# Kernel optimization log

Hardware: AMD Instinct MI355X
Metric: run time of the kernel (lower is better)

The kernel has to match this reference:

```python
import jax, jax.numpy as jnp
import numpy as np

D_MODEL, D_K, D_V, H, D_FF = 512, 64, 64, 8, 2048
B, N = 8, 1024
LN_EPS = 1e-5


def _layer_norm(x, g, b):
    mu = jnp.mean(x, axis=-1, keepdims=True)
    var = jnp.mean((x - mu) ** 2, axis=-1, keepdims=True)
    return (x - mu) * jax.lax.rsqrt(var + LN_EPS) * g + b


def setup_inputs() -> dict:
    key = jax.random.key(0)
    ks = jax.random.split(key, 16)
    s = 0.02
    return {
        "queries": jax.random.normal(ks[0], (B, N, D_MODEL), jnp.float32),
        "keys": jax.random.normal(ks[1], (B, N, D_MODEL), jnp.float32),
        "values": jax.random.normal(ks[2], (B, N, D_MODEL), jnp.float32),
        "relative_geometry_weights": jax.random.uniform(ks[3], (B, H, N, N), jnp.float32),
        "pos": jax.random.normal(ks[4], (B, N, D_MODEL), jnp.float32),
        "Wq": jax.random.normal(ks[5], (D_MODEL, H * D_K), jnp.float32) * s,
        "bq": jnp.zeros((H * D_K,), jnp.float32),
        "Wk": jax.random.normal(ks[6], (D_MODEL, H * D_K), jnp.float32) * s,
        "bk": jnp.zeros((H * D_K,), jnp.float32),
        "Wv": jax.random.normal(ks[7], (D_MODEL, H * D_V), jnp.float32) * s,
        "bv": jnp.zeros((H * D_V,), jnp.float32),
        "Wo": jax.random.normal(ks[8], (H * D_V, D_MODEL), jnp.float32) * s,
        "bo": jnp.zeros((D_MODEL,), jnp.float32),
        "ln1_g": jnp.ones((D_MODEL,), jnp.float32),
        "ln1_b": jnp.zeros((D_MODEL,), jnp.float32),
        "W1": jax.random.normal(ks[9], (D_MODEL, D_FF), jnp.float32) * s,
        "b1": jnp.zeros((D_FF,), jnp.float32),
        "W2": jax.random.normal(ks[10], (D_FF, D_MODEL), jnp.float32) * s,
        "b2": jnp.zeros((D_MODEL,), jnp.float32),
        "ln2_g": jnp.ones((D_MODEL,), jnp.float32),
        "ln2_b": jnp.zeros((D_MODEL,), jnp.float32),
    }


def reference(queries, keys, values, relative_geometry_weights, pos,
              Wq, bq, Wk, bk, Wv, bv, Wo, bo, ln1_g, ln1_b,
              W1, b1, W2, b2, ln2_g, ln2_b):
    b, n, _ = queries.shape
    # positional injection on q/k only
    q_in = queries + pos
    k_in = keys + pos
    # projections -> [b, h, n, d]
    q = (q_in @ Wq + bq).reshape(b, n, H, D_K).transpose(0, 2, 1, 3)
    k = (k_in @ Wk + bk).reshape(b, n, H, D_K).transpose(0, 2, 1, 3)
    v = (values @ Wv + bv).reshape(b, n, H, D_V).transpose(0, 2, 1, 3)
    # scaled dot-product scores with geometry bias: log(clamp(w_g)) + scores
    att = jnp.einsum('bhqd,bhkd->bhqk', q, k) / jnp.sqrt(jnp.float32(D_K))
    w_mn = jnp.log(jnp.clip(relative_geometry_weights, 1e-6, None)) + att
    w_mn = jax.nn.softmax(w_mn, axis=-1)
    out = jnp.einsum('bhqk,bhkd->bhqd', w_mn, v)  # [b,h,n,d_v]
    out = out.transpose(0, 2, 1, 3).reshape(b, n, H * D_V) @ Wo + bo
    # residual + layernorm (dropout is identity in eval)
    att_out = _layer_norm(queries + out, ln1_g, ln1_b)
    # position-wise FFN with residual + layernorm
    ff = jax.nn.relu(att_out @ W1 + b1) @ W2 + b2
    return _layer_norm(att_out + ff, ln2_g, ln2_b)
```

## Files before the change

### kernel.cpp

```cpp
#include <hip/hip_runtime.h>
#include <hip/hip_bf16.h>
#include <stdint.h>

#define B_   8
#define N_   1024
#define DM   512
#define H_   8
#define DFF  2048
#define ROWS (B_ * N_)
#define QKV_LD (3 * DM)
#define LOG2E 1.4426950408889634f
#define SCL  (0.125f * LOG2E)

typedef __bf16 bf16x8 __attribute__((ext_vector_type(8)));
typedef float  f32x4  __attribute__((ext_vector_type(4)));

__device__ __forceinline__ void gld_lds16(const void* g, void* l) {
  __builtin_amdgcn_global_load_lds((__attribute__((address_space(1))) void*)g,
                                   (__attribute__((address_space(3))) void*)l, 16, 0, 0);
}

__device__ __forceinline__ unsigned short bfb(float x) {
  __bf16 h = (__bf16)x;
  unsigned short u;
  __builtin_memcpy(&u, &h, 2);
  return u;
}

__global__ __launch_bounds__(256) void prep_and_wt(
    const float* __restrict__ q, const float* __restrict__ k,
    const float* __restrict__ v, const float* __restrict__ pos,
    __bf16* __restrict__ xq, __bf16* __restrict__ xk, __bf16* __restrict__ xv,
    const float* __restrict__ Wq, const float* __restrict__ Wk,
    const float* __restrict__ Wv, const float* __restrict__ Wo,
    const float* __restrict__ W1, const float* __restrict__ W2,
    __bf16* __restrict__ WqkvT, __bf16* __restrict__ WoT,
    __bf16* __restrict__ W1T, __bf16* __restrict__ W2T) {
  __shared__ float tl[32][33];
  if (blockIdx.x < 4096) {
    int i = blockIdx.x * 256 + threadIdx.x;
    float4 pv = ((const float4*)pos)[i];
    float4 qv = ((const float4*)q)[i];
    float4 kv = ((const float4*)k)[i];
    float4 vv = ((const float4*)v)[i];
    ushort4 o;
    o.x = bfb(qv.x + pv.x); o.y = bfb(qv.y + pv.y); o.z = bfb(qv.z + pv.z); o.w = bfb(qv.w + pv.w);
    ((ushort4*)xq)[i] = o;
    o.x = bfb(kv.x + pv.x); o.y = bfb(kv.y + pv.y); o.z = bfb(kv.z + pv.z); o.w = bfb(kv.w + pv.w);
    ((ushort4*)xk)[i] = o;
    o.x = bfb(vv.x); o.y = bfb(vv.y); o.z = bfb(vv.z); o.w = bfb(vv.w);
    ((ushort4*)xv)[i] = o;
    return;
  }
  int idx = blockIdx.x - 4096;
  const float* src; __bf16* dst; int K, N, t;
  if (idx < 768) {
    src = idx < 256 ? Wq : (idx < 512 ? Wk : Wv);
    dst = WqkvT + (size_t)(idx >> 8) * 512 * 512;
    K = 512; N = 512; t = idx & 255;
  } else if (idx < 1024) { src = Wo; dst = WoT;  K = 512;  N = 512;  t = idx - 768; }
  else if (idx < 2048)   { src = W1; dst = W1T;  K = 512;  N = 2048; t = idx - 1024; }
  else                   { src = W2; dst = W2T;  K = 2048; N = 512;  t = idx - 2048; }
  int tiles_n = N >> 5;
  int tn = t & (tiles_n - 1), tk = t / tiles_n;
  int n0 = tn * 32, k0 = tk * 32;
  int x = threadIdx.x & 31, y4 = threadIdx.x >> 5;
  #pragma unroll
  for (int j = y4; j < 32; j += 8) tl[j][x] = src[(size_t)(k0 + j) * N + n0 + x];
  __syncthreads();
  #pragma unroll
  for (int j = y4; j < 32; j += 8)
    dst[(size_t)(n0 + j) * K + k0 + x] = (__bf16)tl[x][j];
}

template <int EPI, int BN>
__global__ __launch_bounds__(256, 2) void gemm_bt(
    const __bf16* __restrict__ A0, const __bf16* __restrict__ A1, const __bf16* __restrict__ A2,
    const __bf16* __restrict__ BT,
    const float* __restrict__ bias0, const float* __restrict__ bias1, const float* __restrict__ bias2,
    void* __restrict__ Cp, __bf16* __restrict__ Vtp, int M, int N, int K, int nsplit) {
  constexpr int NFR = BN / 32;
  constexpr int WCW = BN / 2;
  constexpr int BI  = BN / 32;
  __shared__ __align__(16) __bf16 As[2][128 * 64];
  __shared__ __align__(16) __bf16 Bs[2][BN * 64];
  int tid = threadIdx.x, lane = tid & 63;
  int wave = tid >> 6;
  int wr = (wave >> 1) * 64, wc = (wave & 1) * WCW;

  int gx = N / BN;
  int nwg = gridDim.x;
  int cpx = nwg >> 3;
  int swz = (blockIdx.x & 7) * cpx + (blockIdx.x >> 3);
  int bx = swz % gx, by = swz / gx;
  int row0 = by << 7, col0 = bx * BN;

  int asel = col0 / nsplit;
  const __bf16* A = asel == 0 ? A0 : (asel == 1 ? A1 : A2);
  const float* bias = asel == 0 ? bias0 : (asel == 1 ? bias1 : bias2);

  f32x4 acc[4][NFR] = {};

#define GSTAGE(BUF, KT)                                                        \
  { _Pragma("unroll")                                                          \
    for (int i = 0; i < 4; ++i) {                                              \
      int t = i * 256 + tid;                                                   \
      int r = t >> 3, cS = (t & 7) ^ (r & 7);                                  \
      gld_lds16(A + (size_t)(row0 + r) * K + (KT) + cS * 8, As[BUF] + t * 8);  \
    }                                                                          \
    _Pragma("unroll")                                                          \
    for (int i = 0; i < BI; ++i) {                                             \
      int t = i * 256 + tid;                                                   \
      int r = t >> 3, cS = (t & 7) ^ (r & 7);                                  \
      gld_lds16(BT + (size_t)(col0 + r) * K + (KT) + cS * 8, Bs[BUF] + t * 8); \
    } }

#define GCOMP(BUF)                                                             \
  { const __bf16* Asc = As[BUF];                                               \
    const __bf16* Bsc = Bs[BUF];                                               \
    _Pragma("unroll")                                                          \
    for (int ks = 0; ks < 2; ++ks) {                                           \
      bf16x8 af[4], bfr[NFR];                                                  \
      _Pragma("unroll")                                                        \
      for (int m = 0; m < 4; ++m) {                                            \
        int r = wr + m * 16 + (lane & 15);                                     \
        int c = (ks * 4 + (lane >> 4)) ^ (r & 7);                              \
        af[m] = *(const bf16x8*)(Asc + r * 64 + c * 8);                        \
      }                                                                        \
      _Pragma("unroll")                                                        \
      for (int n = 0; n < NFR; ++n) {                                          \
        int r = wc + n * 16 + (lane & 15);                                     \
        int c = (ks * 4 + (lane >> 4)) ^ (r & 7);                              \
        bfr[n] = *(const bf16x8*)(Bsc + r * 64 + c * 8);                       \
      }                                                                        \
      _Pragma("unroll")                                                        \
      for (int m = 0; m < 4; ++m)                                              \
        _Pragma("unroll")                                                      \
        for (int n = 0; n < NFR; ++n)                                          \
          acc[m][n] = __builtin_amdgcn_mfma_f32_16x16x32_bf16(af[m], bfr[n], acc[m][n], 0, 0, 0); \
    } }

  GSTAGE(0, 0)
  int cur = 0;
  for (int kt = 64; kt < K; kt += 64) {
    GSTAGE(cur ^ 1, kt)
    if constexpr (BN == 128) asm volatile("s_waitcnt vmcnt(8)" ::: "memory");
    else                     asm volatile("s_waitcnt vmcnt(6)" ::: "memory");
    __builtin_amdgcn_s_barrier();
    __builtin_amdgcn_sched_barrier(0);
    GCOMP(cur)
    __builtin_amdgcn_s_barrier();
    cur ^= 1;
  }
  asm volatile("s_waitcnt vmcnt(0)" ::: "memory");
  __builtin_amdgcn_s_barrier();
  __builtin_amdgcn_sched_barrier(0);
  GCOMP(cur)
#undef GSTAGE
#undef GCOMP

  int rb = row0 + wr + ((lane >> 4) << 2);
  int cb = col0 + wc + (lane & 15);
  if (EPI == 3 && asel == 2) {
    int bb = row0 >> 10;
    #pragma unroll
    for (int n = 0; n < NFR; ++n) {
      int c = cb + n * 16;
      int d = c & 63, hh = (c >> 6) & 7;
      float bv = bias[c % nsplit];
      size_t vbase = ((size_t)((bb * 8 + hh) * 64 + d)) << 10;
      #pragma unroll
      for (int m = 0; m < 4; ++m) {
        int r0 = (rb + m * 16) & 1023;
        ushort4 pk;
        pk.x = bfb(acc[m][n][0] + bv);
        pk.y = bfb(acc[m][n][1] + bv);
        pk.z = bfb(acc[m][n][2] + bv);
        pk.w = bfb(acc[m][n][3] + bv);
        *(ushort4*)((__bf16*)Vtp + vbase + r0) = pk;
      }
    }
    return;
  }
  #pragma unroll
  for (int n = 0; n < NFR; ++n) {
    int c = cb + n * 16;
    float bv = bias[c % nsplit];
    #pragma unroll
    for (int m = 0; m < 4; ++m) {
      #pragma unroll
      for (int j = 0; j < 4; ++j) {
        int r = rb + m * 16 + j;
        float v = acc[m][n][j] + bv;
        if (EPI == 1) v = fmaxf(v, 0.f);
        if (EPI == 2) ((float*)Cp)[(size_t)r * N + c] = v;
        else          ((__bf16*)Cp)[(size_t)r * N + c] = (__bf16)v;
      }
    }
  }
}

__global__ __launch_bounds__(256, 3) void attn_kernel(
    const __bf16* __restrict__ QKV, const __bf16* __restrict__ Vt,
    const float* __restrict__ rgw, __bf16* __restrict__ O) {
  __shared__ __align__(16) __bf16 Qs[64 * 64];
  __shared__ __align__(16) __bf16 Ks[2][64 * 64];
  __shared__ __align__(16) __bf16 Vs[2][64 * 64];
  __shared__ __align__(16) __bf16 Ps[4][16 * 64];

  int tid = threadIdx.x, lane = tid & 63, wave = tid >> 6;
  int flat = (blockIdx.x & 7) * 128 + (blockIdx.x >> 3);
  int qt = flat & 15, h = (flat >> 4) & 7, b = flat >> 7;
  int q0 = qt * 64;
  const int g = lane >> 4, u = lane & 15;

  const float* rgw_p = rgw +
      ((size_t)(b * H_ + h) * N_ + (size_t)(q0 + wave * 16 + u)) * N_ + g * 4;

#define STAGE_KV(BUF, KT)                                                      \
  {                                                                            \
    _Pragma("unroll")                                                          \
    for (int i = 0; i < 2; ++i) {                                              \
      int t = i * 256 + tid;                                                   \
      int r = t >> 3, cL = t & 7, cS = cL ^ (r & 7);                           \
      gld_lds16(QKV + (size_t)(b * N_ + (KT) + r) * QKV_LD + DM + h * 64 + cS * 8, Ks[BUF] + t * 8); \
      gld_lds16(Vt + (size_t)((b * H_ + h) * 64 + r) * N_ + (KT) + cS * 8, Vs[BUF] + t * 8);         \
    }                                                                          \
  }
#define RPF(W, T)                                                              \
  {                                                                            \
    _Pragma("unroll")                                                          \
    for (int n = 0; n < 4; ++n)                                                \
      W[n] = __builtin_nontemporal_load((const f32x4*)(rgw_p + (size_t)(T) * 64 + n * 16)); \
  }

  #pragma unroll
  for (int i = 0; i < 2; ++i) {
    int t = i * 256 + tid;
    int r = t >> 3, cL = t & 7, cS = cL ^ (r & 7);
    gld_lds16(QKV + (size_t)(b * N_ + q0 + r) * QKV_LD + h * 64 + cS * 8, Qs + t * 8);
  }
  STAGE_KV(0, 0)
  __builtin_amdgcn_sched_barrier(0);
  f32x4 wA[4], wB[4], wC[4], wD[4];
  RPF(wA, 0) RPF(wB, 1) RPF(wC, 2)
  __builtin_amdgcn_sched_barrier(0);

  float l = 0.f;
  f32x4 oacc[4] = {};
  bf16x8 qf[2];
  __bf16* pw = &Ps[wave][0];

  union Pk { __bf16 h4[4]; unsigned long long q; };

#define PHASE(T16, WAITSTR, DOSTAGE, DORPF, WCON, WPF)                         \
  {                                                                            \
    asm volatile(WAITSTR ::: "memory");                                        \
    __builtin_amdgcn_s_barrier();                                              \
    if (DOSTAGE) { STAGE_KV(((T16) + 1) & 1, ((T16) + 1) * 64) }               \
    __builtin_amdgcn_sched_barrier(0);                                         \
    if (DORPF) { RPF(WPF, (T16) + 3) }                                         \
    __builtin_amdgcn_sched_barrier(0);                                         \
    if ((T16) == 0) {                                                          \
      int r = wave * 16 + u;                                                   \
      _Pragma("unroll")                                                        \
      for (int ks = 0; ks < 2; ++ks) {                                         \
        int c = (ks * 4 + g) ^ (r & 7);                                        \
        qf[ks] = *(const bf16x8*)(Qs + r * 64 + c * 8);                        \
      }                                                                        \
    }                                                                          \
    f32x4 s[4] = {};                                                           \
    __builtin_amdgcn_s_setprio(1);                                             \
    _Pragma("unroll")                                                          \
    for (int ks = 0; ks < 2; ++ks) {                                           \
      _Pragma("unroll")                                                        \
      for (int n = 0; n < 4; ++n) {                                            \
        int r = n * 16 + u;                                                    \
        int c = (ks * 4 + g) ^ (r & 7);                                        \
        bf16x8 kf = *(const bf16x8*)(Ks[(T16) & 1] + r * 64 + c * 8);          \
        s[n] = __builtin_amdgcn_mfma_f32_16x16x32_bf16(kf, qf[ks], s[n], 0, 0, 0); \
      }                                                                        \
    }                                                                          \
    __builtin_amdgcn_s_setprio(0);                                             \
    _Pragma("unroll")                                                          \
    for (int n = 0; n < 4; ++n) {                                              \
      Pk pk;                                                                   \
      _Pragma("unroll")                                                        \
      for (int j = 0; j < 4; ++j) {                                            \
        float pv = fmaxf(WCON[n][j], 1e-6f) * exp2f(s[n][j] * SCL);            \
        l += pv;                                                               \
        pk.h4[j] = (__bf16)pv;                                                 \
      }                                                                        \
      int bcol = 2 * n + (g >> 1);                                             \
      *(unsigned long long*)(pw + u * 64 + ((bcol ^ (u & 7)) << 3) + ((g & 1) << 2)) = pk.q; \
    }                                                                          \
    __builtin_amdgcn_s_setprio(1);                                             \
    _Pragma("unroll")                                                          \
    for (int ks = 0; ks < 2; ++ks) {                                           \
      int cp = (ks * 4 + g) ^ (u & 7);                                         \
      bf16x8 pa = *(const bf16x8*)(pw + u * 64 + cp * 8);                      \
      _Pragma("unroll")                                                        \
      for (int n = 0; n < 4; ++n) {                                            \
        int r = n * 16 + u;                                                    \
        int c = (ks * 4 + g) ^ (r & 7);                                        \
        bf16x8 vb = *(const bf16x8*)(Vs[(T16) & 1] + r * 64 + c * 8);          \
        oacc[n] = __builtin_amdgcn_mfma_f32_16x16x32_bf16(pa, vb, oacc[n], 0, 0, 0); \
      }                                                                        \
    }                                                                          \
    __builtin_amdgcn_s_setprio(0);                                             \
  }

  PHASE(0,  "s_waitcnt vmcnt(12)", 1, 1, wA, wD)
  PHASE(1,  "s_waitcnt vmcnt(4)",  1, 1, wB, wA)
  PHASE(2,  "s_waitcnt vmcnt(4)",  1, 1, wC, wB)
  PHASE(3,  "s_waitcnt vmcnt(4)",  1, 1, wD, wC)
  PHASE(4,  "s_waitcnt vmcnt(4)",  1, 1, wA, wD)
  PHASE(5,  "s_waitcnt vmcnt(4)",  1, 1, wB, wA)
  PHASE(6,  "s_waitcnt vmcnt(4)",  1, 1, wC, wB)
  PHASE(7,  "s_waitcnt vmcnt(4)",  1, 1, wD, wC)
  PHASE(8,  "s_waitcnt vmcnt(4)",  1, 1, wA, wD)
  PHASE(9,  "s_waitcnt vmcnt(4)",  1, 1, wB, wA)
  PHASE(10, "s_waitcnt vmcnt(4)",  1, 1, wC, wB)
  PHASE(11, "s_waitcnt vmcnt(4)",  1, 1, wD, wC)
  PHASE(12, "s_waitcnt vmcnt(4)",  1, 1, wA, wD)
  PHASE(13, "s_waitcnt vmcnt(4)",  1, 0, wB, wA)
  PHASE(14, "s_waitcnt vmcnt(0)",  1, 0, wC, wB)
  PHASE(15, "s_waitcnt vmcnt(0)",  0, 0, wD, wC)
#undef PHASE
#undef STAGE_KV
#undef RPF

  l += __shfl_xor(l, 16);
  l += __shfl_xor(l, 32);
  float linv[4];
  #pragma unroll
  for (int j = 0; j < 4; ++j)
    linv[j] = 1.f / __shfl(l, (lane & 48) | (g * 4 + j));

  int orow = b * N_ + q0 + wave * 16 + g * 4;
  int ocol = h * 64 + u;
  #pragma unroll
  for (int j = 0; j < 4; ++j)
    #pragma unroll
    for (int n = 0; n < 4; ++n)
      O[(size_t)(orow + j) * DM + ocol + n * 16] = (__bf16)(oacc[n][j] * linv[j]);
}

template <int WRITE_BF>
__global__ __launch_bounds__(256) void ln_kernel(
    const float* __restrict__ x1, const float* __restrict__ x2,
    const float* __restrict__ gw, const float* __restrict__ bw,
    float* __restrict__ outf, __bf16* __restrict__ outb) {
  __shared__ float red[8];
  int row = blockIdx.x, t = threadIdx.x;
  size_t base = (size_t)row * DM;
  float v0 = x1[base + t] + x2[base + t];
  float v1 = x1[base + t + 256] + x2[base + t + 256];
  float s = v0 + v1, s2 = v0 * v0 + v1 * v1;
  #pragma unroll
  for (int o = 32; o; o >>= 1) { s += __shfl_xor(s, o); s2 += __shfl_xor(s2, o); }
  int wave = t >> 6;
  if ((t & 63) == 0) { red[wave] = s; red[4 + wave] = s2; }
  __syncthreads();
  s = red[0] + red[1] + red[2] + red[3];
  s2 = red[4] + red[5] + red[6] + red[7];
  float mu = s * (1.f / DM);
  float var = s2 * (1.f / DM) - mu * mu;
  float rstd = rsqrtf(var + 1e-5f);
  float y0 = (v0 - mu) * rstd * gw[t] + bw[t];
  float y1 = (v1 - mu) * rstd * gw[t + 256] + bw[t + 256];
  outf[base + t] = y0;
  outf[base + t + 256] = y1;
  if (WRITE_BF) {
    outb[base + t] = (__bf16)y0;
    outb[base + t + 256] = (__bf16)y1;
  }
}

extern "C" void kernel_launch(void* const* d_in, const int* in_sizes, int n_in,
                              void* d_out, int out_size, void* d_ws, size_t ws_size,
                              hipStream_t stream) {
  const float* queries = (const float*)d_in[0];
  const float* keys    = (const float*)d_in[1];
  const float* values  = (const float*)d_in[2];
  const float* rgw     = (const float*)d_in[3];
  const float* pos     = (const float*)d_in[4];
  const float* Wq = (const float*)d_in[5];
  const float* bq = (const float*)d_in[6];
  const float* Wk = (const float*)d_in[7];
  const float* bk = (const float*)d_in[8];
  const float* Wv = (const float*)d_in[9];
  const float* bv = (const float*)d_in[10];
  const float* Wo = (const float*)d_in[11];
  const float* bo = (const float*)d_in[12];
  const float* ln1g = (const float*)d_in[13];
  const float* ln1b = (const float*)d_in[14];
  const float* W1 = (const float*)d_in[15];
  const float* b1 = (const float*)d_in[16];
  const float* W2 = (const float*)d_in[17];
  const float* b2 = (const float*)d_in[18];
  const float* ln2g = (const float*)d_in[19];
  const float* ln2b = (const float*)d_in[20];
  float* out = (float*)d_out;

  char* ws = (char*)d_ws;
  const size_t SZX = (size_t)ROWS * DM * 2;
  __bf16* Xq    = (__bf16*)(ws);
  __bf16* Xk    = (__bf16*)(ws + SZX);
  __bf16* Xv    = (__bf16*)(ws + 2 * SZX);
  __bf16* WqkvT = (__bf16*)(ws + 3 * SZX);
  __bf16* WoT   = (__bf16*)(ws + 3 * SZX + 1572864);
  __bf16* W1T   = (__bf16*)(ws + 3 * SZX + 2097152);
  __bf16* W2T   = (__bf16*)(ws + 3 * SZX + 4194304);
  __bf16* QKV   = (__bf16*)(ws + 3 * SZX + 6291456);
  __bf16* Vt    = (__bf16*)(ws + 3 * SZX + 6291456 + 3 * SZX);
  __bf16* Oat   = (__bf16*)(ws + 3 * SZX + 6291456 + 4 * SZX);
  float*  attproj = (float*)Xq;
  __bf16* attoutb = Xv;
  float*  attoutf = (float*)QKV;
  float*  ff2     = (float*)Vt;
  __bf16* ff1     = (__bf16*)(ws + 3 * SZX + 6291456 + 5 * SZX);

  prep_and_wt<<<4096 + 3072, 256, 0, stream>>>(
      queries, keys, values, pos, Xq, Xk, Xv,
      Wq, Wk, Wv, Wo, W1, W2, WqkvT, WoT, W1T, W2T);

  gemm_bt<3, 128><<<(ROWS / 128) * (QKV_LD / 128), 256, 0, stream>>>(
      Xq, Xk, Xv, WqkvT, bq, bk, bv, QKV, Vt, ROWS, QKV_LD, DM, DM);

  attn_kernel<<<B_ * H_ * (N_ / 64), 256, 0, stream>>>(QKV, Vt, rgw, Oat);

  gemm_bt<2, 64><<<(ROWS / 128) * (DM / 64), 256, 0, stream>>>(
      Oat, Oat, Oat, WoT, bo, bo, bo, attproj, nullptr, ROWS, DM, DM, DM);

  ln_kernel<1><<<ROWS, 256, 0, stream>>>(queries, attproj, ln1g, ln1b, attoutf, attoutb);

  gemm_bt<1, 128><<<(ROWS / 128) * (DFF / 128), 256, 0, stream>>>(
      attoutb, attoutb, attoutb, W1T, b1, b1, b1, ff1, nullptr, ROWS, DFF, DM, DFF);

  gemm_bt<2, 64><<<(ROWS / 128) * (DM / 64), 256, 0, stream>>>(
      ff1, ff1, ff1, W2T, b2, b2, b2, ff2, nullptr, ROWS, DM, DFF, DM);

  ln_kernel<0><<<ROWS, 256, 0, stream>>>(attoutf, ff2, ln2g, ln2b, out, nullptr);
}
```

Baseline: 223.9 us.

## Process 128 query rows per attention block and store GEMM outputs as bf16

The attention kernel now handles two 64-row query tiles per block, reusing each staged K/V tile for both and halving K/V global traffic. The geometry-weight prefetch becomes double-buffered per tile, and occupancy drops to 2 blocks per SM. The output-projection and FFN2 GEMMs now write bf16 instead of fp32, and layernorm reads the bf16 residual input with vectorized float2 loads and stores. This cuts intermediate memory traffic at the cost of extra rounding before layernorm.

```diff
diff --git a/kernel.cpp b/kernel.cpp
--- a/kernel.cpp
+++ b/kernel.cpp
@@ -200,22 +200,23 @@
   }
 }
 
-__global__ __launch_bounds__(256, 3) void attn_kernel(
+__global__ __launch_bounds__(256, 2) void attn_kernel(
     const __bf16* __restrict__ QKV, const __bf16* __restrict__ Vt,
     const float* __restrict__ rgw, __bf16* __restrict__ O) {
-  __shared__ __align__(16) __bf16 Qs[64 * 64];
+  __shared__ __align__(16) __bf16 Qs[128 * 64];
   __shared__ __align__(16) __bf16 Ks[2][64 * 64];
   __shared__ __align__(16) __bf16 Vs[2][64 * 64];
   __shared__ __align__(16) __bf16 Ps[4][16 * 64];
 
   int tid = threadIdx.x, lane = tid & 63, wave = tid >> 6;
-  int flat = (blockIdx.x & 7) * 128 + (blockIdx.x >> 3);
-  int qt = flat & 15, h = (flat >> 4) & 7, b = flat >> 7;
-  int q0 = qt * 64;
+  int flat = (blockIdx.x & 7) * 64 + (blockIdx.x >> 3);
+  int qt = flat & 7, h = (flat >> 3) & 7, b = flat >> 6;
+  int q0 = qt * 128;
   const int g = lane >> 4, u = lane & 15;
 
-  const float* rgw_p = rgw +
+  const float* rgw_p0 = rgw +
       ((size_t)(b * H_ + h) * N_ + (size_t)(q0 + wave * 16 + u)) * N_ + g * 4;
+  const float* rgw_p1 = rgw_p0 + (size_t)64 * N_;
 
 #define STAGE_KV(BUF, KT)                                                      \
   {                                                                            \
@@ -227,135 +228,160 @@
       gld_lds16(Vt + (size_t)((b * H_ + h) * 64 + r) * N_ + (KT) + cS * 8, Vs[BUF] + t * 8);         \
     }                                                                          \
   }
-#define RPF(W, T)                                                              \
+#define RPF(W, P, T)                                                           \
   {                                                                            \
     _Pragma("unroll")                                                          \
     for (int n = 0; n < 4; ++n)                                                \
-      W[n] = __builtin_nontemporal_load((const f32x4*)(rgw_p + (size_t)(T) * 64 + n * 16)); \
-  }
-
-  #pragma unroll
-  for (int i = 0; i < 2; ++i) {
+      W[n] = __builtin_nontemporal_load((const f32x4*)((P) + (size_t)(T) * 64 + n * 16)); \
+  }
+
+  #pragma unroll
+  for (int i = 0; i < 4; ++i) {
     int t = i * 256 + tid;
     int r = t >> 3, cL = t & 7, cS = cL ^ (r & 7);
     gld_lds16(QKV + (size_t)(b * N_ + q0 + r) * QKV_LD + h * 64 + cS * 8, Qs + t * 8);
   }
   STAGE_KV(0, 0)
   __builtin_amdgcn_sched_barrier(0);
-  f32x4 wA[4], wB[4], wC[4], wD[4];
-  RPF(wA, 0) RPF(wB, 1) RPF(wC, 2)
+  f32x4 wA0[4], wA1[4], wB0[4], wB1[4];
+  RPF(wA0, rgw_p0, 0) RPF(wA1, rgw_p1, 0)
+  RPF(wB0, rgw_p0, 1) RPF(wB1, rgw_p1, 1)
   __builtin_amdgcn_sched_barrier(0);
 
-  float l = 0.f;
-  f32x4 oacc[4] = {};
-  bf16x8 qf[2];
+  float l0 = 0.f, l1 = 0.f;
+  f32x4 oacc0[4] = {}, oacc1[4] = {};
+  bf16x8 qf0[2], qf1[2];
   __bf16* pw = &Ps[wave][0];
 
   union Pk { __bf16 h4[4]; unsigned long long q; };
 
-#define PHASE(T16, WAITSTR, DOSTAGE, DORPF, WCON, WPF)                         \
+#define TILE_ONE(T, CUR, QF, WC, RGWP, OA, LREF, DORPF)                        \
+  {                                                                            \
+    f32x4 s[4] = {};                                                           \
+    __builtin_amdgcn_s_setprio(1);                                             \
+    _Pragma("unroll")                                                          \
+    for (int ks = 0; ks < 2; ++ks) {                                           \
+      _Pragma("unroll")                                                        \
+      for (int n = 0; n < 4; ++n) {                                            \
+        int r = n * 16 + u;                                                    \
+        int c = (ks * 4 + g) ^ (r & 7);                                        \
+        bf16x8 kf = *(const bf16x8*)(Ks[CUR] + r * 64 + c * 8);                \
+        s[n] = __builtin_amdgcn_mfma_f32_16x16x32_bf16(kf, QF[ks], s[n], 0, 0, 0); \
+      }                                                                        \
+    }                                                                          \
+    __builtin_amdgcn_s_setprio(0);                                             \
+    _Pragma("unroll")                                                          \
+    for (int n = 0; n < 4; ++n) {                                              \
+      Pk pk;                                                                   \
+      _Pragma("unroll")                                                        \
+      for (int j = 0; j < 4; ++j) {                                            \
+        float pv = fmaxf(WC[n][j], 1e-6f) * exp2f(s[n][j] * SCL);              \
+        LREF += pv;                                                            \
+        pk.h4[j] = (__bf16)pv;                                                 \
+      }                                                                        \
+      int bcol = 2 * n + (g >> 1);                                             \
+      *(unsigned long long*)(pw + u * 64 + ((bcol ^ (u & 7)) << 3) + ((g & 1) << 2)) = pk.q; \
+    }                                                                          \
+    __builtin_amdgcn_sched_barrier(0);                                         \
+    if (DORPF) { RPF(WC, RGWP, (T) + 2) }                                      \
+    __builtin_amdgcn_sched_barrier(0);                                         \
+    __builtin_amdgcn_s_setprio(1);                                             \
+    _Pragma("unroll")                                                          \
+    for (int ks = 0; ks < 2; ++ks) {                                           \
+      int cp = (ks * 4 + g) ^ (u & 7);                                         \
+      bf16x8 pa = *(const bf16x8*)(pw + u * 64 + cp * 8);                      \
+      _Pragma("unroll")                                                        \
+      for (int n = 0; n < 4; ++n) {                                            \
+        int r = n * 16 + u;                                                    \
+        int c = (ks * 4 + g) ^ (r & 7);                                        \
+        bf16x8 vb = *(const bf16x8*)(Vs[CUR] + r * 64 + c * 8);                \
+        OA[n] = __builtin_amdgcn_mfma_f32_16x16x32_bf16(pa, vb, OA[n], 0, 0, 0); \
+      }                                                                        \
+    }                                                                          \
+    __builtin_amdgcn_s_setprio(0);                                             \
+  }
+
+#define PHASE(T16, WAITSTR, DOSTAGE, DORPF, W0, W1)                            \
   {                                                                            \
     asm volatile(WAITSTR ::: "memory");                                        \
     __builtin_amdgcn_s_barrier();                                              \
     if (DOSTAGE) { STAGE_KV(((T16) + 1) & 1, ((T16) + 1) * 64) }               \
     __builtin_amdgcn_sched_barrier(0);                                         \
-    if (DORPF) { RPF(WPF, (T16) + 3) }                                         \
-    __builtin_amdgcn_sched_barrier(0);                                         \
     if ((T16) == 0) {                                                          \
       int r = wave * 16 + u;                                                   \
       _Pragma("unroll")                                                        \
       for (int ks = 0; ks < 2; ++ks) {                                         \
         int c = (ks * 4 + g) ^ (r & 7);                                        \
-        qf[ks] = *(const bf16x8*)(Qs + r * 64 + c * 8);                        \
-      }                                                                        \
-    }                                                                          \
-    f32x4 s[4] = {};                                                           \
-    __builtin_amdgcn_s_setprio(1);                                             \
-    _Pragma("unroll")                                                          \
-    for (int ks = 0; ks < 2; ++ks) {                                           \
-      _Pragma("unroll")                                                        \
-      for (int n = 0; n < 4; ++n) {                                            \
-        int r = n * 16 + u;                                                    \
-        int c = (ks * 4 + g) ^ (r & 7);                                        \
-        bf16x8 kf = *(const bf16x8*)(Ks[(T16) & 1] + r * 64 + c * 8);          \
-        s[n] = __builtin_amdgcn_mfma_f32_16x16x32_bf16(kf, qf[ks], s[n], 0, 0, 0); \
-      }                                                                        \
-    }                                                                          \
-    __builtin_amdgcn_s_setprio(0);                                             \
-    _Pragma("unroll")                                                          \
-    for (int n = 0; n < 4; ++n) {                                              \
-      Pk pk;                                                                   \
-      _Pragma("unroll")                                                        \
-      for (int j = 0; j < 4; ++j) {                                            \
-        float pv = fmaxf(WCON[n][j], 1e-6f) * exp2f(s[n][j] * SCL);            \
-        l += pv;                                                               \
-        pk.h4[j] = (__bf16)pv;                                                 \
-      }                                                                        \
-      int bcol = 2 * n + (g >> 1);                                             \
-      *(unsigned long long*)(pw + u * 64 + ((bcol ^ (u & 7)) << 3) + ((g & 1) << 2)) = pk.q; \
-    }                                                                          \
-    __builtin_amdgcn_s_setprio(1);                                             \
-    _Pragma("unroll")                                                          \
-    for (int ks = 0; ks < 2; ++ks) {                                           \
-      int cp = (ks * 4 + g) ^ (u & 7);                                         \
-      bf16x8 pa = *(const bf16x8*)(pw + u * 64 + cp * 8);                      \
-      _Pragma("unroll")                                                        \
-      for (int n = 0; n < 4; ++n) {                                            \
-        int r = n * 16 + u;                                                    \
-        int c = (ks * 4 + g) ^ (r & 7);                                        \
-        bf16x8 vb = *(const bf16x8*)(Vs[(T16) & 1] + r * 64 + c * 8);          \
-        oacc[n] = __builtin_amdgcn_mfma_f32_16x16x32_bf16(pa, vb, oacc[n], 0, 0, 0); \
-      }                                                                        \
-    }                                                                          \
-    __builtin_amdgcn_s_setprio(0);                                             \
-  }
-
-  PHASE(0,  "s_waitcnt vmcnt(12)", 1, 1, wA, wD)
-  PHASE(1,  "s_waitcnt vmcnt(4)",  1, 1, wB, wA)
-  PHASE(2,  "s_waitcnt vmcnt(4)",  1, 1, wC, wB)
-  PHASE(3,  "s_waitcnt vmcnt(4)",  1, 1, wD, wC)
-  PHASE(4,  "s_waitcnt vmcnt(4)",  1, 1, wA, wD)
-  PHASE(5,  "s_waitcnt vmcnt(4)",  1, 1, wB, wA)
-  PHASE(6,  "s_waitcnt vmcnt(4)",  1, 1, wC, wB)
-  PHASE(7,  "s_waitcnt vmcnt(4)",  1, 1, wD, wC)
-  PHASE(8,  "s_waitcnt vmcnt(4)",  1, 1, wA, wD)
-  PHASE(9,  "s_waitcnt vmcnt(4)",  1, 1, wB, wA)
-  PHASE(10, "s_waitcnt vmcnt(4)",  1, 1, wC, wB)
-  PHASE(11, "s_waitcnt vmcnt(4)",  1, 1, wD, wC)
-  PHASE(12, "s_waitcnt vmcnt(4)",  1, 1, wA, wD)
-  PHASE(13, "s_waitcnt vmcnt(4)",  1, 0, wB, wA)
-  PHASE(14, "s_waitcnt vmcnt(0)",  1, 0, wC, wB)
-  PHASE(15, "s_waitcnt vmcnt(0)",  0, 0, wD, wC)
+        qf0[ks] = *(const bf16x8*)(Qs + r * 64 + c * 8);                       \
+        qf1[ks] = *(const bf16x8*)(Qs + (64 + r) * 64 + c * 8);                \
+      }                                                                        \
+    }                                                                          \
+    TILE_ONE(T16, (T16) & 1, qf0, W0, rgw_p0, oacc0, l0, DORPF)                \
+    TILE_ONE(T16, (T16) & 1, qf1, W1, rgw_p1, oacc1, l1, DORPF)                \
+  }
+
+  PHASE(0,  "s_waitcnt vmcnt(16)", 1, 1, wA0, wA1)
+  PHASE(1,  "s_waitcnt vmcnt(8)",  1, 1, wB0, wB1)
+  PHASE(2,  "s_waitcnt vmcnt(8)",  1, 1, wA0, wA1)
+  PHASE(3,  "s_waitcnt vmcnt(8)",  1, 1, wB0, wB1)
+  PHASE(4,  "s_waitcnt vmcnt(8)",  1, 1, wA0, wA1)
+  PHASE(5,  "s_waitcnt vmcnt(8)",  1, 1, wB0, wB1)
+  PHASE(6,  "s_waitcnt vmcnt(8)",  1, 1, wA0, wA1)
+  PHASE(7,  "s_waitcnt vmcnt(8)",  1, 1, wB0, wB1)
+  PHASE(8,  "s_waitcnt vmcnt(8)",  1, 1, wA0, wA1)
+  PHASE(9,  "s_waitcnt vmcnt(8)",  1, 1, wB0, wB1)
+  PHASE(10, "s_waitcnt vmcnt(8)",  1, 1, wA0, wA1)
+  PHASE(11, "s_waitcnt vmcnt(8)",  1, 1, wB0, wB1)
+  PHASE(12, "s_waitcnt vmcnt(8)",  1, 1, wA0, wA1)
+  PHASE(13, "s_waitcnt vmcnt(8)",  1, 1, wB0, wB1)
+  PHASE(14, "s_waitcnt vmcnt(8)",  1, 0, wA0, wA1)
+  PHASE(15, "s_waitcnt vmcnt(0)",  0, 0, wB0, wB1)
 #undef PHASE
+#undef TILE_ONE
 #undef STAGE_KV
 #undef RPF
 
-  l += __shfl_xor(l, 16);
-  l += __shfl_xor(l, 32);
-  float linv[4];
-  #pragma unroll
-  for (int j = 0; j < 4; ++j)
-    linv[j] = 1.f / __shfl(l, (lane & 48) | (g * 4 + j));
+  l0 += __shfl_xor(l0, 16); l0 += __shfl_xor(l0, 32);
+  l1 += __shfl_xor(l1, 16); l1 += __shfl_xor(l1, 32);
+  float linv0[4], linv1[4];
+  #pragma unroll
+  for (int j = 0; j < 4; ++j) {
+    int src = (lane & 48) | (g * 4 + j);
+    linv0[j] = 1.f / __shfl(l0, src);
+    linv1[j] = 1.f / __shfl(l1, src);
+  }
 
   int orow = b * N_ + q0 + wave * 16 + g * 4;
   int ocol = h * 64 + u;
   #pragma unroll
   for (int j = 0; j < 4; ++j)
     #pragma unroll
-    for (int n = 0; n < 4; ++n)
-      O[(size_t)(orow + j) * DM + ocol + n * 16] = (__bf16)(oacc[n][j] * linv[j]);
-}
-
-template <int WRITE_BF>
+    for (int n = 0; n < 4; ++n) {
+      O[(size_t)(orow + j) * DM + ocol + n * 16] = (__bf16)(oacc0[n][j] * linv0[j]);
+      O[(size_t)(orow + 64 + j) * DM + ocol + n * 16] = (__bf16)(oacc1[n][j] * linv1[j]);
+    }
+}
+
+template <int WRITE_BF, int X2BF>
 __global__ __launch_bounds__(256) void ln_kernel(
-    const float* __restrict__ x1, const float* __restrict__ x2,
+    const float* __restrict__ x1, const void* __restrict__ x2v,
     const float* __restrict__ gw, const float* __restrict__ bw,
     float* __restrict__ outf, __bf16* __restrict__ outb) {
   __shared__ float red[8];
   int row = blockIdx.x, t = threadIdx.x;
   size_t base = (size_t)row * DM;
-  float v0 = x1[base + t] + x2[base + t];
-  float v1 = x1[base + t + 256] + x2[base + t + 256];
+  float2 a = ((const float2*)(x1 + base))[t];
+  float b0, b1;
+  if (X2BF) {
+    unsigned p = ((const unsigned*)x2v)[base / 2 + t];
+    union { unsigned u; float f; } c0, c1;
+    c0.u = p << 16; c1.u = p & 0xffff0000u;
+    b0 = c0.f; b1 = c1.f;
+  } else {
+    float2 bb = ((const float2*)x2v)[base / 2 + t];
+    b0 = bb.x; b1 = bb.y;
+  }
+  float v0 = a.x + b0, v1 = a.y + b1;
   float s = v0 + v1, s2 = v0 * v0 + v1 * v1;
   #pragma unroll
   for (int o = 32; o; o >>= 1) { s += __shfl_xor(s, o); s2 += __shfl_xor(s2, o); }
@@ -367,13 +393,13 @@
   float mu = s * (1.f / DM);
   float var = s2 * (1.f / DM) - mu * mu;
   float rstd = rsqrtf(var + 1e-5f);
-  float y0 = (v0 - mu) * rstd * gw[t] + bw[t];
-  float y1 = (v1 - mu) * rstd * gw[t + 256] + bw[t + 256];
-  outf[base + t] = y0;
-  outf[base + t + 256] = y1;
+  float y0 = (v0 - mu) * rstd * gw[2 * t] + bw[2 * t];
+  float y1 = (v1 - mu) * rstd * gw[2 * t + 1] + bw[2 * t + 1];
+  float2 r; r.x = y0; r.y = y1;
+  ((float2*)(outf + base))[t] = r;
   if (WRITE_BF) {
-    outb[base + t] = (__bf16)y0;
-    outb[base + t + 256] = (__bf16)y1;
+    ushort2 h; h.x = bfb(y0); h.y = bfb(y1);
+    ((ushort2*)(outb + base))[t] = h;
   }
 }
 
@@ -415,11 +441,11 @@
   __bf16* QKV   = (__bf16*)(ws + 3 * SZX + 6291456);
   __bf16* Vt    = (__bf16*)(ws + 3 * SZX + 6291456 + 3 * SZX);
   __bf16* Oat   = (__bf16*)(ws + 3 * SZX + 6291456 + 4 * SZX);
-  float*  attproj = (float*)Xq;
-  __bf16* attoutb = Xv;
-  float*  attoutf = (float*)QKV;
-  float*  ff2     = (float*)Vt;
-  __bf16* ff1     = (__bf16*)(ws + 3 * SZX + 6291456 + 5 * SZX);
+  __bf16* attprojb = Xq;
+  __bf16* attoutb  = Xv;
+  float*  attoutf  = (float*)QKV;
+  __bf16* ff2b     = Vt;
+  __bf16* ff1      = (__bf16*)(ws + 3 * SZX + 6291456 + 5 * SZX);
 
   prep_and_wt<<<4096 + 3072, 256, 0, stream>>>(
       queries, keys, values, pos, Xq, Xk, Xv,
@@ -428,18 +454,18 @@
   gemm_bt<3, 128><<<(ROWS / 128) * (QKV_LD / 128), 256, 0, stream>>>(
       Xq, Xk, Xv, WqkvT, bq, bk, bv, QKV, Vt, ROWS, QKV_LD, DM, DM);
 
-  attn_kernel<<<B_ * H_ * (N_ / 64), 256, 0, stream>>>(QKV, Vt, rgw, Oat);
-
-  gemm_bt<2, 64><<<(ROWS / 128) * (DM / 64), 256, 0, stream>>>(
-      Oat, Oat, Oat, WoT, bo, bo, bo, attproj, nullptr, ROWS, DM, DM, DM);
-
-  ln_kernel<1><<<ROWS, 256, 0, stream>>>(queries, attproj, ln1g, ln1b, attoutf, attoutb);
+  attn_kernel<<<B_ * H_ * (N_ / 128), 256, 0, stream>>>(QKV, Vt, rgw, Oat);
+
+  gemm_bt<0, 64><<<(ROWS / 128) * (DM / 64), 256, 0, stream>>>(
+      Oat, Oat, Oat, WoT, bo, bo, bo, attprojb, nullptr, ROWS, DM, DM, DM);
+
+  ln_kernel<1, 1><<<ROWS, 256, 0, stream>>>(queries, attprojb, ln1g, ln1b, attoutf, attoutb);
 
   gemm_bt<1, 128><<<(ROWS / 128) * (DFF / 128), 256, 0, stream>>>(
       attoutb, attoutb, attoutb, W1T, b1, b1, b1, ff1, nullptr, ROWS, DFF, DM, DFF);
 
-  gemm_bt<2, 64><<<(ROWS / 128) * (DM / 64), 256, 0, stream>>>(
-      ff1, ff1, ff1, W2T, b2, b2, b2, ff2, nullptr, ROWS, DM, DFF, DM);
-
-  ln_kernel<0><<<ROWS, 256, 0, stream>>>(attoutf, ff2, ln2g, ln2b, out, nullptr);
-}
+  gemm_bt<0, 64><<<(ROWS / 128) * (DM / 64), 256, 0, stream>>>(
+      ff1, ff1, ff1, W2T, b2, b2, b2, ff2b, nullptr, ROWS, DM, DFF, DM);
+
+  ln_kernel<0, 1><<<ROWS, 256, 0, stream>>>(attoutf, ff2b, ln2g, ln2b, out, nullptr);
+}
```

Measured after the change: 210.6 us. 1.06x faster.

## Stage geometry weights through LDS and switch GEMM outputs to bf16 before layernorm

Applied to the files above, without the earlier changes.

The attention kernel now loads the relative-geometry weight tiles into double-buffered shared memory with async global-to-LDS copies. This replaces the per-thread register prefetch ring with its staggered waitcnts, and waits fully at each phase. Occupancy is lowered to 2 blocks per CU to fit the extra 32KB of LDS. Separately, the Wo and W2 GEMMs write bf16 instead of fp32, and the layernorm kernels read them with vectorized float2/bf16x2 accesses, which halves the intermediate traffic at some precision cost.

```diff
diff --git a/kernel.cpp b/kernel.cpp
--- a/kernel.cpp
+++ b/kernel.cpp
@@ -200,12 +200,13 @@
   }
 }
 
-__global__ __launch_bounds__(256, 3) void attn_kernel(
+__global__ __launch_bounds__(256, 2) void attn_kernel(
     const __bf16* __restrict__ QKV, const __bf16* __restrict__ Vt,
     const float* __restrict__ rgw, __bf16* __restrict__ O) {
   __shared__ __align__(16) __bf16 Qs[64 * 64];
   __shared__ __align__(16) __bf16 Ks[2][64 * 64];
   __shared__ __align__(16) __bf16 Vs[2][64 * 64];
+  __shared__ __align__(16) float  Ws[2][64 * 64];
   __shared__ __align__(16) __bf16 Ps[4][16 * 64];
 
   int tid = threadIdx.x, lane = tid & 63, wave = tid >> 6;
@@ -214,59 +215,52 @@
   int q0 = qt * 64;
   const int g = lane >> 4, u = lane & 15;
 
-  const float* rgw_p = rgw +
-      ((size_t)(b * H_ + h) * N_ + (size_t)(q0 + wave * 16 + u)) * N_ + g * 4;
-
-#define STAGE_KV(BUF, KT)                                                      \
+  size_t wbase = ((size_t)(b * H_ + h) * N_ + (size_t)q0) * N_;
+
+#define STAGE_T(BUF, KT)                                                       \
   {                                                                            \
     _Pragma("unroll")                                                          \
     for (int i = 0; i < 2; ++i) {                                              \
       int t = i * 256 + tid;                                                   \
-      int r = t >> 3, cL = t & 7, cS = cL ^ (r & 7);                           \
+      int r = t >> 3, cS = (t & 7) ^ (r & 7);                                  \
       gld_lds16(QKV + (size_t)(b * N_ + (KT) + r) * QKV_LD + DM + h * 64 + cS * 8, Ks[BUF] + t * 8); \
       gld_lds16(Vt + (size_t)((b * H_ + h) * 64 + r) * N_ + (KT) + cS * 8, Vs[BUF] + t * 8);         \
     }                                                                          \
-  }
-#define RPF(W, T)                                                              \
-  {                                                                            \
-    _Pragma("unroll")                                                          \
-    for (int n = 0; n < 4; ++n)                                                \
-      W[n] = __builtin_nontemporal_load((const f32x4*)(rgw_p + (size_t)(T) * 64 + n * 16)); \
+    _Pragma("unroll")                                                          \
+    for (int i = 0; i < 4; ++i) {                                              \
+      int C = i * 256 + tid;                            \
+      int R = C >> 4, c = C & 15;                                              \
+      int sc = (c ^ (R & 7)) << 2;       \
+      gld_lds16(rgw + wbase + (size_t)R * N_ + (KT) + sc, Ws[BUF] + C * 4);    \
+    }                                                                          \
   }
 
   #pragma unroll
   for (int i = 0; i < 2; ++i) {
     int t = i * 256 + tid;
-    int r = t >> 3, cL = t & 7, cS = cL ^ (r & 7);
+    int r = t >> 3, cS = (t & 7) ^ (r & 7);
     gld_lds16(QKV + (size_t)(b * N_ + q0 + r) * QKV_LD + h * 64 + cS * 8, Qs + t * 8);
   }
-  STAGE_KV(0, 0)
-  __builtin_amdgcn_sched_barrier(0);
-  f32x4 wA[4], wB[4], wC[4], wD[4];
-  RPF(wA, 0) RPF(wB, 1) RPF(wC, 2)
-  __builtin_amdgcn_sched_barrier(0);
+  STAGE_T(0, 0)
 
   float l = 0.f;
   f32x4 oacc[4] = {};
   bf16x8 qf[2];
   __bf16* pw = &Ps[wave][0];
-
+  const int wrow = wave * 16 + u;
   union Pk { __bf16 h4[4]; unsigned long long q; };
 
-#define PHASE(T16, WAITSTR, DOSTAGE, DORPF, WCON, WPF)                         \
+#define PHASE(T16, DOSTAGE)                                                    \
   {                                                                            \
-    asm volatile(WAITSTR ::: "memory");                                        \
+    asm volatile("s_waitcnt vmcnt(0)" ::: "memory");                           \
     __builtin_amdgcn_s_barrier();                                              \
-    if (DOSTAGE) { STAGE_KV(((T16) + 1) & 1, ((T16) + 1) * 64) }               \
-    __builtin_amdgcn_sched_barrier(0);                                         \
-    if (DORPF) { RPF(WPF, (T16) + 3) }                                         \
+    if (DOSTAGE) { STAGE_T(((T16) + 1) & 1, ((T16) + 1) * 64) }                \
     __builtin_amdgcn_sched_barrier(0);                                         \
     if ((T16) == 0) {                                                          \
-      int r = wave * 16 + u;                                                   \
       _Pragma("unroll")                                                        \
       for (int ks = 0; ks < 2; ++ks) {                                         \
-        int c = (ks * 4 + g) ^ (r & 7);                                        \
-        qf[ks] = *(const bf16x8*)(Qs + r * 64 + c * 8);                        \
+        int c = (ks * 4 + g) ^ (wrow & 7);                                     \
+        qf[ks] = *(const bf16x8*)(Qs + wrow * 64 + c * 8);                     \
       }                                                                        \
     }                                                                          \
     f32x4 s[4] = {};                                                           \
@@ -282,12 +276,17 @@
       }                                                                        \
     }                                                                          \
     __builtin_amdgcn_s_setprio(0);                                             \
+                        \
+    f32x4 w[4];                                                                \
+    _Pragma("unroll")                                                          \
+    for (int n = 0; n < 4; ++n)                                                \
+      w[n] = *(const f32x4*)(Ws[(T16) & 1] + wrow * 64 + (((4 * n + g) ^ (u & 7)) << 2)); \
     _Pragma("unroll")                                                          \
     for (int n = 0; n < 4; ++n) {                                              \
       Pk pk;                                                                   \
       _Pragma("unroll")                                                        \
       for (int j = 0; j < 4; ++j) {                                            \
-        float pv = fmaxf(WCON[n][j], 1e-6f) * exp2f(s[n][j] * SCL);            \
+        float pv = fmaxf(w[n][j], 1e-6f) * exp2f(s[n][j] * SCL);               \
         l += pv;                                                               \
         pk.h4[j] = (__bf16)pv;                                                 \
       }                                                                        \
@@ -310,25 +309,12 @@
     __builtin_amdgcn_s_setprio(0);                                             \
   }
 
-  PHASE(0,  "s_waitcnt vmcnt(12)", 1, 1, wA, wD)
-  PHASE(1,  "s_waitcnt vmcnt(4)",  1, 1, wB, wA)
-  PHASE(2,  "s_waitcnt vmcnt(4)",  1, 1, wC, wB)
-  PHASE(3,  "s_waitcnt vmcnt(4)",  1, 1, wD, wC)
-  PHASE(4,  "s_waitcnt vmcnt(4)",  1, 1, wA, wD)
-  PHASE(5,  "s_waitcnt vmcnt(4)",  1, 1, wB, wA)
-  PHASE(6,  "s_waitcnt vmcnt(4)",  1, 1, wC, wB)
-  PHASE(7,  "s_waitcnt vmcnt(4)",  1, 1, wD, wC)
-  PHASE(8,  "s_waitcnt vmcnt(4)",  1, 1, wA, wD)
-  PHASE(9,  "s_waitcnt vmcnt(4)",  1, 1, wB, wA)
-  PHASE(10, "s_waitcnt vmcnt(4)",  1, 1, wC, wB)
-  PHASE(11, "s_waitcnt vmcnt(4)",  1, 1, wD, wC)
-  PHASE(12, "s_waitcnt vmcnt(4)",  1, 1, wA, wD)
-  PHASE(13, "s_waitcnt vmcnt(4)",  1, 0, wB, wA)
-  PHASE(14, "s_waitcnt vmcnt(0)",  1, 0, wC, wB)
-  PHASE(15, "s_waitcnt vmcnt(0)",  0, 0, wD, wC)
+  PHASE(0, 1)  PHASE(1, 1)  PHASE(2, 1)  PHASE(3, 1)
+  PHASE(4, 1)  PHASE(5, 1)  PHASE(6, 1)  PHASE(7, 1)
+  PHASE(8, 1)  PHASE(9, 1)  PHASE(10, 1) PHASE(11, 1)
+  PHASE(12, 1) PHASE(13, 1) PHASE(14, 1) PHASE(15, 0)
 #undef PHASE
-#undef STAGE_KV
-#undef RPF
+#undef STAGE_T
 
   l += __shfl_xor(l, 16);
   l += __shfl_xor(l, 32);
@@ -346,16 +332,26 @@
       O[(size_t)(orow + j) * DM + ocol + n * 16] = (__bf16)(oacc[n][j] * linv[j]);
 }
 
-template <int WRITE_BF>
+template <int WRITE_BF, int X2BF>
 __global__ __launch_bounds__(256) void ln_kernel(
-    const float* __restrict__ x1, const float* __restrict__ x2,
+    const float* __restrict__ x1, const void* __restrict__ x2v,
     const float* __restrict__ gw, const float* __restrict__ bw,
     float* __restrict__ outf, __bf16* __restrict__ outb) {
   __shared__ float red[8];
   int row = blockIdx.x, t = threadIdx.x;
   size_t base = (size_t)row * DM;
-  float v0 = x1[base + t] + x2[base + t];
-  float v1 = x1[base + t + 256] + x2[base + t + 256];
+  float2 a = ((const float2*)(x1 + base))[t];
+  float b0, b1;
+  if (X2BF) {
+    unsigned p = ((const unsigned*)x2v)[base / 2 + t];
+    union { unsigned u; float f; } c0, c1;
+    c0.u = p << 16; c1.u = p & 0xffff0000u;
+    b0 = c0.f; b1 = c1.f;
+  } else {
+    float2 bb = ((const float2*)x2v)[base / 2 + t];
+    b0 = bb.x; b1 = bb.y;
+  }
+  float v0 = a.x + b0, v1 = a.y + b1;
   float s = v0 + v1, s2 = v0 * v0 + v1 * v1;
   #pragma unroll
   for (int o = 32; o; o >>= 1) { s += __shfl_xor(s, o); s2 += __shfl_xor(s2, o); }
@@ -367,13 +363,13 @@
   float mu = s * (1.f / DM);
   float var = s2 * (1.f / DM) - mu * mu;
   float rstd = rsqrtf(var + 1e-5f);
-  float y0 = (v0 - mu) * rstd * gw[t] + bw[t];
-  float y1 = (v1 - mu) * rstd * gw[t + 256] + bw[t + 256];
-  outf[base + t] = y0;
-  outf[base + t + 256] = y1;
+  float y0 = (v0 - mu) * rstd * gw[2 * t] + bw[2 * t];
+  float y1 = (v1 - mu) * rstd * gw[2 * t + 1] + bw[2 * t + 1];
+  float2 r; r.x = y0; r.y = y1;
+  ((float2*)(outf + base))[t] = r;
   if (WRITE_BF) {
-    outb[base + t] = (__bf16)y0;
-    outb[base + t + 256] = (__bf16)y1;
+    ushort2 h; h.x = bfb(y0); h.y = bfb(y1);
+    ((ushort2*)(outb + base))[t] = h;
   }
 }
 
@@ -415,11 +411,11 @@
   __bf16* QKV   = (__bf16*)(ws + 3 * SZX + 6291456);
   __bf16* Vt    = (__bf16*)(ws + 3 * SZX + 6291456 + 3 * SZX);
   __bf16* Oat   = (__bf16*)(ws + 3 * SZX + 6291456 + 4 * SZX);
-  float*  attproj = (float*)Xq;
-  __bf16* attoutb = Xv;
-  float*  attoutf = (float*)QKV;
-  float*  ff2     = (float*)Vt;
-  __bf16* ff1     = (__bf16*)(ws + 3 * SZX + 6291456 + 5 * SZX);
+  __bf16* attprojb = Xq;
+  __bf16* attoutb  = Xv;
+  float*  attoutf  = (float*)QKV;
+  __bf16* ff2b     = Vt;
+  __bf16* ff1      = (__bf16*)(ws + 3 * SZX + 6291456 + 5 * SZX);
 
   prep_and_wt<<<4096 + 3072, 256, 0, stream>>>(
       queries, keys, values, pos, Xq, Xk, Xv,
@@ -430,16 +426,16 @@
 
   attn_kernel<<<B_ * H_ * (N_ / 64), 256, 0, stream>>>(QKV, Vt, rgw, Oat);
 
-  gemm_bt<2, 64><<<(ROWS / 128) * (DM / 64), 256, 0, stream>>>(
-      Oat, Oat, Oat, WoT, bo, bo, bo, attproj, nullptr, ROWS, DM, DM, DM);
-
-  ln_kernel<1><<<ROWS, 256, 0, stream>>>(queries, attproj, ln1g, ln1b, attoutf, attoutb);
+  gemm_bt<0, 64><<<(ROWS / 128) * (DM / 64), 256, 0, stream>>>(
+      Oat, Oat, Oat, WoT, bo, bo, bo, attprojb, nullptr, ROWS, DM, DM, DM);
+
+  ln_kernel<1, 1><<<ROWS, 256, 0, stream>>>(queries, attprojb, ln1g, ln1b, attoutf, attoutb);
 
   gemm_bt<1, 128><<<(ROWS / 128) * (DFF / 128), 256, 0, stream>>>(
       attoutb, attoutb, attoutb, W1T, b1, b1, b1, ff1, nullptr, ROWS, DFF, DM, DFF);
 
-  gemm_bt<2, 64><<<(ROWS / 128) * (DM / 64), 256, 0, stream>>>(
-      ff1, ff1, ff1, W2T, b2, b2, b2, ff2, nullptr, ROWS, DM, DFF, DM);
-
-  ln_kernel<0><<<ROWS, 256, 0, stream>>>(attoutf, ff2, ln2g, ln2b, out, nullptr);
-}
+  gemm_bt<0, 64><<<(ROWS / 128) * (DM / 64), 256, 0, stream>>>(
+      ff1, ff1, ff1, W2T, b2, b2, b2, ff2b, nullptr, ROWS, DM, DFF, DM);
+
+  ln_kernel<0, 1><<<ROWS, 256, 0, stream>>>(attoutf, ff2b, ln2g, ln2b, out, nullptr);
+}
```

Result: no change. 223.9 us (-0.0%).
